# Performance work log

Hardware: AMD Instinct MI355X
Metric: run time of the kernel (lower is better)

Reference implementation:

```python
import jax, jax.numpy as jnp
import numpy as np

B, S, H = 2, 2048, 1024
NH, HD = 16, 64


def setup_inputs() -> dict:
    key = jax.random.key(0)
    ks = jax.random.split(key, 6)
    sc = 0.02
    return {
        "hidden_states": jax.random.normal(ks[0], (B, S, H), dtype=jnp.float32),
        "attention_mask": jnp.zeros((B, 1, 1, S), dtype=jnp.float32),
        "rel_pos": jax.random.normal(ks[1], (B, NH, S, S), dtype=jnp.float32) * 0.1,
        "Wq": jax.random.normal(ks[2], (H, H), dtype=jnp.float32) * sc,
        "bq": jnp.zeros((H,), dtype=jnp.float32),
        "Wk": jax.random.normal(ks[3], (H, H), dtype=jnp.float32) * sc,
        "bk": jnp.zeros((H,), dtype=jnp.float32),
        "Wv": jax.random.normal(ks[4], (H, H), dtype=jnp.float32) * sc,
        "bv": jnp.zeros((H,), dtype=jnp.float32),
    }


def reference(hidden_states, attention_mask, rel_pos, Wq, bq, Wk, bk, Wv, bv):
    def heads(x):  # [B,S,H] -> [B,NH,S,HD]
        return x.reshape(B, S, NH, HD).transpose(0, 2, 1, 3)

    q = heads(hidden_states @ Wq.T + bq)
    k = heads(hidden_states @ Wk.T + bk)
    v = heads(hidden_states @ Wv.T + bv)

    scores = jnp.einsum('bhqd,bhkd->bhqk', q, k) / jnp.sqrt(jnp.float32(HD))
    scores = scores + attention_mask + rel_pos
    probs = jax.nn.softmax(scores, axis=-1)
    ctx = jnp.einsum('bhqk,bhkd->bhqd', probs, v)
    return ctx.transpose(0, 2, 1, 3).reshape(B, S, H)
```

## Files before the change

kernel.cpp:

```cpp
#include <hip/hip_runtime.h>
#include <hip/hip_bf16.h>

#define B_  2
#define S_  2048
#define H_  1024
#define NH_ 16
#define HD_ 64

typedef __bf16 bf16_t;
typedef __attribute__((ext_vector_type(4))) __bf16 bf16x4;
typedef __attribute__((ext_vector_type(8))) __bf16 bf16x8;
typedef __attribute__((ext_vector_type(4))) float f32x4;

__device__ __forceinline__ void gld_lds16(const bf16_t* g, bf16_t* l) {
    __builtin_amdgcn_global_load_lds(
        (const __attribute__((address_space(1))) unsigned int*)g,
        (__attribute__((address_space(3))) unsigned int*)l, 16, 0, 0);
}

__global__ __launch_bounds__(256) void cast_bf16(
    const float* __restrict__ X, const float* __restrict__ Wq,
    const float* __restrict__ Wk, const float* __restrict__ Wv,
    bf16_t* __restrict__ Xb, bf16_t* __restrict__ Wb)
{
    const size_t XN = (size_t)B_ * S_ * H_;
    size_t i4 = ((size_t)blockIdx.x * 256 + threadIdx.x) * 4;
    const float* src;
    bf16_t* dst;
    if (i4 < XN) {
        src = X + i4; dst = Xb + i4;
    } else {
        size_t j = i4 - XN;
        int wsel = (int)(j >> 20);
        const float* Wp = wsel == 0 ? Wq : (wsel == 1 ? Wk : Wv);
        src = Wp + (j & 1048575); dst = Wb + j;
    }
    float4 v = *(const float4*)src;
    bf16x4 o = { (bf16_t)v.x, (bf16_t)v.y, (bf16_t)v.z, (bf16_t)v.w };
    *(bf16x4*)dst = o;
}

__global__ __launch_bounds__(256, 2) void qkv_gemm(
    const bf16_t* __restrict__ Xb, const bf16_t* __restrict__ Wb,
    const float* __restrict__ bq, const float* __restrict__ bk,
    const float* __restrict__ bv,
    bf16_t* __restrict__ qbuf, bf16_t* __restrict__ kbuf, bf16_t* __restrict__ vbuf)
{
    const int which = blockIdx.z;
    const bf16_t* W  = Wb + (size_t)which * H_ * H_;
    const float* bias = which == 0 ? bq : (which == 1 ? bk : bv);
    bf16_t* out       = which == 0 ? qbuf : (which == 1 ? kbuf : vbuf);
    const float scale = which == 0 ? 0.125f : 1.0f;

    const int m0 = blockIdx.x * 128;
    const int n0 = blockIdx.y * 128;
    const int t    = threadIdx.x;
    const int lane = t & 63;
    const int w    = t >> 6;
    const int wr   = w >> 1, wc = w & 1;
    const int lo   = lane & 15, g = lane >> 4;

    __shared__ bf16_t As[2][128 * 64];
    __shared__ bf16_t Bs[2][128 * 64];

    const int srow = w * 8 + (lane >> 3);
    const int scol = (lane & 7) * 8;
    const bf16_t* ga = Xb + (size_t)(m0 + srow) * H_ + scol;
    const bf16_t* gb = W  + (size_t)(n0 + srow) * H_ + scol;

    f32x4 acc[4][4];
#pragma unroll
    for (int mt = 0; mt < 4; ++mt)
#pragma unroll
        for (int nt = 0; nt < 4; ++nt)
            acc[mt][nt] = (f32x4){0.f, 0.f, 0.f, 0.f};

#pragma unroll
    for (int p = 0; p < 4; ++p) {
        gld_lds16(ga + (size_t)p * 32 * H_, &As[0][p * 2048 + w * 512]);
        gld_lds16(gb + (size_t)p * 32 * H_, &Bs[0][p * 2048 + w * 512]);
    }
    asm volatile("s_waitcnt vmcnt(0)" ::: "memory");
    __builtin_amdgcn_s_barrier();

    for (int kc = 0; kc < 16; ++kc) {
        const int cur = kc & 1;
        if (kc < 15) {
#pragma unroll
            for (int p = 0; p < 4; ++p) {
                gld_lds16(ga + (size_t)p * 32 * H_ + (kc + 1) * 64,
                          &As[cur ^ 1][p * 2048 + w * 512]);
                gld_lds16(gb + (size_t)p * 32 * H_ + (kc + 1) * 64,
                          &Bs[cur ^ 1][p * 2048 + w * 512]);
            }
        }

        bf16x8 a0[4], a1[4];
#pragma unroll
        for (int mt = 0; mt < 4; ++mt) {
            a0[mt] = *(const bf16x8*)&As[cur][(wr * 64 + mt * 16 + lo) * 64 + g * 8];
            a1[mt] = *(const bf16x8*)&As[cur][(wr * 64 + mt * 16 + lo) * 64 + g * 8 + 32];
        }
        __builtin_amdgcn_s_setprio(1);
#pragma unroll
        for (int nt = 0; nt < 4; ++nt) {
            bf16x8 b0 = *(const bf16x8*)&Bs[cur][(wc * 64 + nt * 16 + lo) * 64 + g * 8];
            bf16x8 b1 = *(const bf16x8*)&Bs[cur][(wc * 64 + nt * 16 + lo) * 64 + g * 8 + 32];
#pragma unroll
            for (int mt = 0; mt < 4; ++mt) {
                acc[mt][nt] = __builtin_amdgcn_mfma_f32_16x16x32_bf16(a0[mt], b0, acc[mt][nt], 0, 0, 0);
                acc[mt][nt] = __builtin_amdgcn_mfma_f32_16x16x32_bf16(a1[mt], b1, acc[mt][nt], 0, 0, 0);
            }
        }
        __builtin_amdgcn_s_setprio(0);

        if (kc < 15) {
            asm volatile("s_waitcnt vmcnt(0)" ::: "memory");
            __builtin_amdgcn_s_barrier();
        }
    }

#pragma unroll
    for (int nt = 0; nt < 4; ++nt) {
        int n  = n0 + wc * 64 + nt * 16 + lo;
        int hh = n >> 6, d = n & 63;
        float bv_ = bias[n];
#pragma unroll
        for (int mt = 0; mt < 4; ++mt) {
#pragma unroll
            for (int r = 0; r < 4; ++r) {
                int m = m0 + wr * 64 + mt * 16 + g * 4 + r;
                int b = m >> 11, s = m & 2047;
                out[(((size_t)(b * NH_ + hh) * S_) + s) * HD_ + d] =
                    (bf16_t)((acc[mt][nt][r] + bv_) * scale);
            }
        }
    }
}

__global__ __launch_bounds__(256, 2) void attn(
    const bf16_t* __restrict__ qbuf, const bf16_t* __restrict__ kbuf,
    const bf16_t* __restrict__ vbuf,
    const float* __restrict__ mask, const float* __restrict__ rel,
    float* __restrict__ out)
{
    const int bid  = blockIdx.x;
    const int work = ((bid & 7) << 7) | (bid >> 3);
    const int q0 = (work & 31) * 64;
    const int h  = (work >> 5) & 15;
    const int b  = work >> 9;

    const int t    = threadIdx.x;
    const int lane = t & 63;
    const int w    = t >> 6;
    const int lo   = lane & 15;
    const int g    = lane >> 4;

    __shared__ bf16_t QPs[64 * 72];
    __shared__ bf16_t Ks [64 * 72];
    __shared__ bf16_t VTs[64 * 72];
    __shared__ float  Ms [S_];
    __shared__ float  Rs [2][64 * 68];

    const bf16_t* qg = qbuf + ((size_t)(b * NH_ + h) * S_ + q0) * HD_;
    const bf16_t* kg = kbuf + (size_t)(b * NH_ + h) * S_ * HD_;
    const bf16_t* vg = vbuf + (size_t)(b * NH_ + h) * S_ * HD_;
    const float*  relg  = rel + ((size_t)((b * NH_ + h) * S_ + q0)) * S_;
    const float*  maskg = mask + (size_t)b * S_;

    const int r0 = t >> 3;
    const int c8 = (t & 7) * 8;
    const int rrow = t >> 2;
    const int rc16 = (t & 3) * 16;

    uint4 kv0 = *(const uint4*)&kg[(size_t)r0 * 64 + c8];
    uint4 kv1 = *(const uint4*)&kg[(size_t)(r0 + 32) * 64 + c8];
    uint4 vv0 = *(const uint4*)&vg[(size_t)r0 * 64 + c8];
    uint4 vv1 = *(const uint4*)&vg[(size_t)(r0 + 32) * 64 + c8];

    float4 rr[4];
#pragma unroll
    for (int p = 0; p < 4; ++p)
        rr[p] = *(const float4*)&relg[(size_t)rrow * S_ + rc16 + p * 4];

    uint4  qv0 = *(const uint4*)&qg[(size_t)r0 * 64 + c8];
    uint4  qv1 = *(const uint4*)&qg[(size_t)(r0 + 32) * 64 + c8];
    float4 mv0 = *(const float4*)&maskg[t * 8];
    float4 mv1 = *(const float4*)&maskg[t * 8 + 4];

    *(uint4*)&QPs[r0 * 72 + c8]        = qv0;
    *(uint4*)&QPs[(r0 + 32) * 72 + c8] = qv1;
    *(float4*)&Ms[t * 8]     = mv0;
    *(float4*)&Ms[t * 8 + 4] = mv1;

#pragma unroll
    for (int p = 0; p < 4; ++p)
        *(float4*)&Rs[0][rrow * 68 + rc16 + p * 4] = rr[p];
#pragma unroll
    for (int p = 0; p < 4; ++p)
        rr[p] = *(const float4*)&relg[(size_t)rrow * S_ + 64 + rc16 + p * 4];

    asm volatile("s_waitcnt lgkmcnt(0)" ::: "memory");
    __builtin_amdgcn_s_barrier();

    bf16x8 aq0 = *(const bf16x8*)&QPs[(w * 16 + lo) * 72 + g * 8];
    bf16x8 aq1 = *(const bf16x8*)&QPs[(w * 16 + lo) * 72 + g * 8 + 32];

    float mi[4], li[4];
    f32x4 accO[4];
#pragma unroll
    for (int r = 0; r < 4; ++r) { mi[r] = -1e30f; li[r] = 0.f; }
#pragma unroll
    for (int dt = 0; dt < 4; ++dt) accO[dt] = (f32x4){0.f, 0.f, 0.f, 0.f};

    const int qrow = w * 16 + g * 4;

    for (int kc = 0; kc < 32; ++kc) {
        *(uint4*)&Ks[r0 * 72 + c8]        = kv0;
        *(uint4*)&Ks[(r0 + 32) * 72 + c8] = kv1;
        {
            const bf16_t* vp0 = (const bf16_t*)&vv0;
            const bf16_t* vp1 = (const bf16_t*)&vv1;
            int sw0 = r0 ^ c8, sw1 = (r0 + 32) ^ c8;
#pragma unroll
            for (int j = 0; j < 8; ++j) {
                VTs[(c8 + j) * 72 + sw0] = vp0[j];
                VTs[(c8 + j) * 72 + sw1] = vp1[j];
            }
        }
        if (kc < 31) {
            float* Rd = &Rs[(kc + 1) & 1][rrow * 68 + rc16];
#pragma unroll
            for (int p = 0; p < 4; ++p)
                *(float4*)&Rd[p * 4] = rr[p];
            const int kn = (kc + 2 <= 31) ? kc + 2 : 31;
#pragma unroll
            for (int p = 0; p < 4; ++p)
                rr[p] = *(const float4*)&relg[(size_t)rrow * S_ + kn * 64 + rc16 + p * 4];
        }
        {
            const int kn = (kc < 31) ? kc + 1 : kc;
            const bf16_t* kgn = kg + (size_t)kn * 64 * 64;
            const bf16_t* vgn = vg + (size_t)kn * 64 * 64;
            kv0 = *(const uint4*)&kgn[(size_t)r0 * 64 + c8];
            kv1 = *(const uint4*)&kgn[(size_t)(r0 + 32) * 64 + c8];
            vv0 = *(const uint4*)&vgn[(size_t)r0 * 64 + c8];
            vv1 = *(const uint4*)&vgn[(size_t)(r0 + 32) * 64 + c8];
        }

        asm volatile("s_waitcnt lgkmcnt(0)" ::: "memory");
        __builtin_amdgcn_s_barrier();

        f32x4 sc[4];
        __builtin_amdgcn_s_setprio(1);
#pragma unroll
        for (int nt = 0; nt < 4; ++nt) {
            bf16x8 b0 = *(const bf16x8*)&Ks[(nt * 16 + lo) * 72 + g * 8];
            bf16x8 b1 = *(const bf16x8*)&Ks[(nt * 16 + lo) * 72 + g * 8 + 32];
            f32x4 z = (f32x4){0.f, 0.f, 0.f, 0.f};
            z = __builtin_amdgcn_mfma_f32_16x16x32_bf16(aq0, b0, z, 0, 0, 0);
            z = __builtin_amdgcn_mfma_f32_16x16x32_bf16(aq1, b1, z, 0, 0, 0);
            sc[nt] = z;
        }
        __builtin_amdgcn_s_setprio(0);

        const float* Rc = &Rs[kc & 1][0];
        float sv[4][4];
#pragma unroll
        for (int nt = 0; nt < 4; ++nt) {
            float mk = Ms[kc * 64 + nt * 16 + lo];
#pragma unroll
            for (int r = 0; r < 4; ++r)
                sv[r][nt] = sc[nt][r] + mk + Rc[(qrow + r) * 68 + nt * 16 + lo];
        }

        bf16_t* Pw = &QPs[w * 16 * 72];
#pragma unroll
        for (int r = 0; r < 4; ++r) {
            float vmax = fmaxf(fmaxf(sv[r][0], sv[r][1]), fmaxf(sv[r][2], sv[r][3]));
#pragma unroll
            for (int mk2 = 1; mk2 < 16; mk2 <<= 1)
                vmax = fmaxf(vmax, __shfl_xor(vmax, mk2, 16));
            float mnew  = fmaxf(mi[r], vmax);
            float alpha = __expf(mi[r] - mnew);
            float rsum = 0.f;
#pragma unroll
            for (int nt = 0; nt < 4; ++nt) {
                float p = __expf(sv[r][nt] - mnew);
                sv[r][nt] = p;
                rsum += p;
            }
#pragma unroll
            for (int mk2 = 1; mk2 < 16; mk2 <<= 1)
                rsum += __shfl_xor(rsum, mk2, 16);
            li[r] = li[r] * alpha + rsum;
            mi[r] = mnew;
#pragma unroll
            for (int dt = 0; dt < 4; ++dt) accO[dt][r] *= alpha;
#pragma unroll
            for (int nt = 0; nt < 4; ++nt)
                Pw[(g * 4 + r) * 72 + ((nt * 16 + lo) ^ (g * 8))] = (bf16_t)sv[r][nt];
        }

        bf16x8 pa0 = *(const bf16x8*)&Pw[lo * 72 + ((g * 8)       ^ ((lo >> 2) * 8))];
        bf16x8 pa1 = *(const bf16x8*)&Pw[lo * 72 + (((4 + g) * 8) ^ ((lo >> 2) * 8))];
        __builtin_amdgcn_s_setprio(1);
#pragma unroll
        for (int dt = 0; dt < 4; ++dt) {
            int d = dt * 16 + lo;
            bf16x8 v0 = *(const bf16x8*)&VTs[d * 72 + ((g * 8)       ^ (d & 56))];
            bf16x8 v1 = *(const bf16x8*)&VTs[d * 72 + (((4 + g) * 8) ^ (d & 56))];
            accO[dt] = __builtin_amdgcn_mfma_f32_16x16x32_bf16(pa0, v0, accO[dt], 0, 0, 0);
            accO[dt] = __builtin_amdgcn_mfma_f32_16x16x32_bf16(pa1, v1, accO[dt], 0, 0, 0);
        }
        __builtin_amdgcn_s_setprio(0);

        asm volatile("s_waitcnt lgkmcnt(0)" ::: "memory");
        __builtin_amdgcn_s_barrier();
    }

#pragma unroll
    for (int dt = 0; dt < 4; ++dt) {
        int d = dt * 16 + lo;
#pragma unroll
        for (int r = 0; r < 4; ++r) {
            int row = q0 + w * 16 + g * 4 + r;
            out[((size_t)(b * S_ + row)) * H_ + h * HD_ + d] = accO[dt][r] / li[r];
        }
    }
}

extern "C" void kernel_launch(void* const* d_in, const int* in_sizes, int n_in,
                              void* d_out, int out_size, void* d_ws, size_t ws_size,
                              hipStream_t stream) {
    const float* hs   = (const float*)d_in[0];
    const float* mask = (const float*)d_in[1];
    const float* rel  = (const float*)d_in[2];
    const float* Wq   = (const float*)d_in[3];
    const float* bq   = (const float*)d_in[4];
    const float* Wk   = (const float*)d_in[5];
    const float* bk   = (const float*)d_in[6];
    const float* Wv   = (const float*)d_in[7];
    const float* bv   = (const float*)d_in[8];
    float* out = (float*)d_out;

    const size_t qkv_elems = (size_t)B_ * NH_ * S_ * HD_;
    bf16_t* qbuf = (bf16_t*)d_ws;
    bf16_t* kbuf = qbuf + qkv_elems;
    bf16_t* vbuf = kbuf + qkv_elems;
    bf16_t* Xb   = vbuf + qkv_elems;
    bf16_t* Wb   = Xb   + qkv_elems;

    cast_bf16<<<7168, 256, 0, stream>>>(hs, Wq, Wk, Wv, Xb, Wb);
    qkv_gemm<<<dim3(32, 8, 3), 256, 0, stream>>>(Xb, Wb, bq, bk, bv,
                                                 qbuf, kbuf, vbuf);
    attn<<<1024, 256, 0, stream>>>(qbuf, kbuf, vbuf, mask, rel, out);
}
```

Measured before the change: 885.4 us.

## Load rel_pos directly into registers, pack V transpose stores, raise occupancy

Removes the double-buffered LDS staging of the rel_pos tile and has each lane load its own rel_pos values straight from global memory into registers, one chunk ahead of use. Freeing that LDS lets the launch bound request 4 blocks per CU instead of 2. The V transpose now loads pairs of adjacent rows and writes packed 32-bit values with an XOR swizzle, halving the LDS store count. The direct rel_pos loads are scalar and strided per lane rather than coalesced float4, and prefetching one chunk ahead gives less latency cover. The tighter register budget may also cause spills.

New measurement: 817.4 us. -7.7%, faster.

```diff
diff --git a/kernel.cpp b/kernel.cpp
--- a/kernel.cpp
+++ b/kernel.cpp
@@ -138,7 +138,7 @@
     }
 }
 
-__global__ __launch_bounds__(256, 2) void attn(
+__global__ __launch_bounds__(256, 4) void attn(
     const bf16_t* __restrict__ qbuf, const bf16_t* __restrict__ kbuf,
     const bf16_t* __restrict__ vbuf,
     const float* __restrict__ mask, const float* __restrict__ rel,
@@ -160,7 +160,6 @@
     __shared__ bf16_t Ks [64 * 72];
     __shared__ bf16_t VTs[64 * 72];
     __shared__ float  Ms [S_];
-    __shared__ float  Rs [2][64 * 68];
 
     const bf16_t* qg = qbuf + ((size_t)(b * NH_ + h) * S_ + q0) * HD_;
     const bf16_t* kg = kbuf + (size_t)(b * NH_ + h) * S_ * HD_;
@@ -170,36 +169,30 @@
 
     const int r0 = t >> 3;
     const int c8 = (t & 7) * 8;
-    const int rrow = t >> 2;
-    const int rc16 = (t & 3) * 16;
 
     uint4 kv0 = *(const uint4*)&kg[(size_t)r0 * 64 + c8];
     uint4 kv1 = *(const uint4*)&kg[(size_t)(r0 + 32) * 64 + c8];
-    uint4 vv0 = *(const uint4*)&vg[(size_t)r0 * 64 + c8];
-    uint4 vv1 = *(const uint4*)&vg[(size_t)(r0 + 32) * 64 + c8];
-
-    float4 rr[4];
-#pragma unroll
-    for (int p = 0; p < 4; ++p)
-        rr[p] = *(const float4*)&relg[(size_t)rrow * S_ + rc16 + p * 4];
+    uint4 vv0 = *(const uint4*)&vg[(size_t)(2 * r0) * 64 + c8];
+    uint4 vv1 = *(const uint4*)&vg[(size_t)(2 * r0 + 1) * 64 + c8];
 
     uint4  qv0 = *(const uint4*)&qg[(size_t)r0 * 64 + c8];
     uint4  qv1 = *(const uint4*)&qg[(size_t)(r0 + 32) * 64 + c8];
     float4 mv0 = *(const float4*)&maskg[t * 8];
     float4 mv1 = *(const float4*)&maskg[t * 8 + 4];
 
+    const int qrow = w * 16 + g * 4;
+    float rl[4][4];
+#pragma unroll
+    for (int r = 0; r < 4; ++r)
+#pragma unroll
+        for (int nt = 0; nt < 4; ++nt)
+            rl[r][nt] = relg[(size_t)(qrow + r) * S_ + nt * 16 + lo];
+
     *(uint4*)&QPs[r0 * 72 + c8]        = qv0;
     *(uint4*)&QPs[(r0 + 32) * 72 + c8] = qv1;
     *(float4*)&Ms[t * 8]     = mv0;
     *(float4*)&Ms[t * 8 + 4] = mv1;
 
-#pragma unroll
-    for (int p = 0; p < 4; ++p)
-        *(float4*)&Rs[0][rrow * 68 + rc16 + p * 4] = rr[p];
-#pragma unroll
-    for (int p = 0; p < 4; ++p)
-        rr[p] = *(const float4*)&relg[(size_t)rrow * S_ + 64 + rc16 + p * 4];
-
     asm volatile("s_waitcnt lgkmcnt(0)" ::: "memory");
     __builtin_amdgcn_s_barrier();
 
@@ -212,31 +205,20 @@
     for (int r = 0; r < 4; ++r) { mi[r] = -1e30f; li[r] = 0.f; }
 #pragma unroll
     for (int dt = 0; dt < 4; ++dt) accO[dt] = (f32x4){0.f, 0.f, 0.f, 0.f};
-
-    const int qrow = w * 16 + g * 4;
 
     for (int kc = 0; kc < 32; ++kc) {
         *(uint4*)&Ks[r0 * 72 + c8]        = kv0;
         *(uint4*)&Ks[(r0 + 32) * 72 + c8] = kv1;
         {
-            const bf16_t* vp0 = (const bf16_t*)&vv0;
-            const bf16_t* vp1 = (const bf16_t*)&vv1;
-            int sw0 = r0 ^ c8, sw1 = (r0 + 32) ^ c8;
+            const unsigned short* vp0 = (const unsigned short*)&vv0;
+            const unsigned short* vp1 = (const unsigned short*)&vv1;
+            const int s2 = 2 * r0;
 #pragma unroll
             for (int j = 0; j < 8; ++j) {
-                VTs[(c8 + j) * 72 + sw0] = vp0[j];
-                VTs[(c8 + j) * 72 + sw1] = vp1[j];
-            }
-        }
-        if (kc < 31) {
-            float* Rd = &Rs[(kc + 1) & 1][rrow * 68 + rc16];
-#pragma unroll
-            for (int p = 0; p < 4; ++p)
-                *(float4*)&Rd[p * 4] = rr[p];
-            const int kn = (kc + 2 <= 31) ? kc + 2 : 31;
-#pragma unroll
-            for (int p = 0; p < 4; ++p)
-                rr[p] = *(const float4*)&relg[(size_t)rrow * S_ + kn * 64 + rc16 + p * 4];
+                int d = c8 + j;
+                unsigned int pack = (unsigned int)vp0[j] | ((unsigned int)vp1[j] << 16);
+                *(unsigned int*)&VTs[d * 72 + (s2 ^ (d & 56))] = pack;
+            }
         }
         {
             const int kn = (kc < 31) ? kc + 1 : kc;
@@ -244,8 +226,8 @@
             const bf16_t* vgn = vg + (size_t)kn * 64 * 64;
             kv0 = *(const uint4*)&kgn[(size_t)r0 * 64 + c8];
             kv1 = *(const uint4*)&kgn[(size_t)(r0 + 32) * 64 + c8];
-            vv0 = *(const uint4*)&vgn[(size_t)r0 * 64 + c8];
-            vv1 = *(const uint4*)&vgn[(size_t)(r0 + 32) * 64 + c8];
+            vv0 = *(const uint4*)&vgn[(size_t)(2 * r0) * 64 + c8];
+            vv1 = *(const uint4*)&vgn[(size_t)(2 * r0 + 1) * 64 + c8];
         }
 
         asm volatile("s_waitcnt lgkmcnt(0)" ::: "memory");
@@ -264,14 +246,21 @@
         }
         __builtin_amdgcn_s_setprio(0);
 
-        const float* Rc = &Rs[kc & 1][0];
         float sv[4][4];
 #pragma unroll
         for (int nt = 0; nt < 4; ++nt) {
             float mk = Ms[kc * 64 + nt * 16 + lo];
 #pragma unroll
             for (int r = 0; r < 4; ++r)
-                sv[r][nt] = sc[nt][r] + mk + Rc[(qrow + r) * 68 + nt * 16 + lo];
+                sv[r][nt] = sc[nt][r] + mk + rl[r][nt];
+        }
+
+        if (kc < 31) {
+#pragma unroll
+            for (int r = 0; r < 4; ++r)
+#pragma unroll
+                for (int nt = 0; nt < 4; ++nt)
+                    rl[r][nt] = relg[(size_t)(qrow + r) * S_ + (kc + 1) * 64 + nt * 16 + lo];
         }
 
         bf16_t* Pw = &QPs[w * 16 * 72];
```
